# Optimization experiments

Measured on AMD Instinct MI355X. Metric: run time of the kernel, lower is better.

Reference implementation:

```python
import jax, jax.numpy as jnp
import numpy as np

B = 4
NS = [65536, 16384, 4096, 1024, 256]   # nodes per mesh level
DEG = 16                               # avg degree
KORD = 6                               # Chebyshev polynomial order
FE = [3, 16, 16, 16, 32]               # encoder filters
FD = [32, 16, 16, 16, 16, 3]           # decoder filters
Z = 64                                 # latent dim


def cheb_norm(edge_index, n):
    # symmetric normalization D^-1/2 A D^-1/2 per ChebConv_Coma.norm
    row, col = edge_index
    deg = jnp.zeros((n,), jnp.float32).at[row].add(jnp.ones(row.shape, jnp.float32))
    dis = jnp.where(deg > 0, deg ** -0.5, 0.0)
    return dis[row] * dis[col]


def propagate(x, row, col, norm):
    # out[b, row] += norm * x[b, col]   (sparse adjacency matvec, batched)
    return jnp.zeros_like(x).at[:, row].add(x[:, col] * norm[None, :, None])


def cheb_conv(x, edge_index, norm, W, b):
    # Chebyshev recursion: T0 = x, T1 = L x, Tk = 2 L T_{k-1} - T_{k-2}
    row, col = edge_index
    Tx0 = x
    out = jnp.einsum('bnf,fg->bng', Tx0, W[0])
    Tx1 = propagate(x, row, col, norm)
    out = out + jnp.einsum('bnf,fg->bng', Tx1, W[1])
    for k in range(2, W.shape[0]):
        Tx2 = 2.0 * propagate(Tx1, row, col, norm) - Tx0
        out = out + jnp.einsum('bnf,fg->bng', Tx2, W[k])
        Tx0, Tx1 = Tx1, Tx2
    return out + b if b is not None else out


def pool(x, idx, w):
    # sparse pooling matmul: 3 nnz per output row; idx/w: [Nout, 3]
    return jnp.einsum('bnkf,nk->bnf', x[:, idx], w)


def coma_forward(x, eis, dids, dws, uids, uws, encW, encB, decW, decB,
                 enc_w, enc_b, dec_w, dec_b):
    norms = [cheb_norm(eis[i], NS[i]) for i in range(5)]
    h = x.reshape(B, NS[0], FE[0])
    # encoder: cheb conv + relu + downsample pool, 4 levels
    for i in range(4):
        h = jax.nn.relu(cheb_conv(h, eis[i], norms[i], encW[i], encB[i]))
        h = pool(h, dids[i], dws[i])
    h = h.reshape(B, NS[-1] * FE[-1])
    z = jax.nn.relu(h @ enc_w + enc_b)
    # decoder
    h = jax.nn.relu(z @ dec_w + dec_b).reshape(B, NS[-1], FD[0])
    for i in range(4):
        lvl = 3 - i
        h = pool(h, uids[lvl], uws[lvl])
        h = jax.nn.relu(cheb_conv(h, eis[lvl], norms[lvl], decW[i], decB[i]))
    h = cheb_conv(h, eis[0], norms[0], decW[4], None)  # last conv, no bias
    return h.reshape(-1, FE[0])


def setup_inputs() -> dict:
    key = jax.random.key(0)
    ks = iter(jax.random.split(key, 80))
    inp = {}
    inp['x'] = jax.random.normal(next(ks), (B * NS[0], FE[0]), jnp.float32)
    for i, n in enumerate(NS):
        inp[f'ei{i}'] = jax.random.randint(next(ks), (2, DEG * n), 0, n)
    for i in range(4):
        inp[f'down_i{i}'] = jax.random.randint(next(ks), (NS[i + 1], 3), 0, NS[i])
        inp[f'down_w{i}'] = jax.random.uniform(next(ks), (NS[i + 1], 3), jnp.float32)
        inp[f'up_i{i}'] = jax.random.randint(next(ks), (NS[i], 3), 0, NS[i + 1])
        inp[f'up_w{i}'] = jax.random.uniform(next(ks), (NS[i], 3), jnp.float32)
    for i in range(4):
        inp[f'ew{i}'] = 0.1 * jax.random.normal(next(ks), (KORD, FE[i], FE[i + 1]), jnp.float32)
        inp[f'eb{i}'] = jnp.zeros((FE[i + 1],), jnp.float32)
    for i in range(5):
        inp[f'dw{i}'] = 0.1 * jax.random.normal(next(ks), (KORD, FD[i], FD[i + 1]), jnp.float32)
    for i in range(4):
        inp[f'db{i}'] = jnp.zeros((FD[i + 1],), jnp.float32)
    inp['enc_w'] = 0.1 * jax.random.normal(next(ks), (NS[-1] * FE[-1], Z), jnp.float32)
    inp['enc_b'] = 0.1 * jnp.ones((Z,), jnp.float32)
    inp['dec_w'] = 0.1 * jax.random.normal(next(ks), (Z, FD[0] * NS[-1]), jnp.float32)
    inp['dec_b'] = 0.1 * jnp.ones((FD[0] * NS[-1],), jnp.float32)
    return inp


def reference(x, ei0, ei1, ei2, ei3, ei4,
              down_i0, down_w0, up_i0, up_w0,
              down_i1, down_w1, up_i1, up_w1,
              down_i2, down_w2, up_i2, up_w2,
              down_i3, down_w3, up_i3, up_w3,
              ew0, eb0, ew1, eb1, ew2, eb2, ew3, eb3,
              dw0, dw1, dw2, dw3, dw4, db0, db1, db2, db3,
              enc_w, enc_b, dec_w, dec_b):
    eis = [ei0, ei1, ei2, ei3, ei4]
    dids = [down_i0, down_i1, down_i2, down_i3]
    dws = [down_w0, down_w1, down_w2, down_w3]
    uids = [up_i0, up_i1, up_i2, up_i3]
    uws = [up_w0, up_w1, up_w2, up_w3]
    encW = [ew0, ew1, ew2, ew3]
    encB = [eb0, eb1, eb2, eb3]
    decW = [dw0, dw1, dw2, dw3, dw4]
    decB = [db0, db1, db2, db3]
    return coma_forward(x, eis, dids, dws, uids, uws, encW, encB, decW, decB,
                        enc_w, enc_b, dec_w, dec_b)
```

## Files before the change

### kernel.cpp

```cpp
#include <hip/hip_runtime.h>

#define TPB 256

static constexpr int B_ = 4;
static constexpr int DEG_ = 16;

using u16 = unsigned short;

static constexpr int LB0 = 0, LB1 = 65536, LB2 = 81920, LB3 = 86016, LB4 = 87040;
static constexpr int CE0 = 0, CE1 = 1048576, CE2 = 1310720, CE3 = 1376256, CE4 = 1392640;


__device__ inline float b2f(u16 u) { return __uint_as_float((unsigned)u << 16); }
__device__ inline u16 f2b(float f) {
    unsigned b = __float_as_uint(f);
    b += 0x7fffu + ((b >> 16) & 1u);
    return (u16)(b >> 16);
}

template<int F>
__device__ inline void load_row_bf16(const u16* __restrict__ p, float* v) {
    if constexpr (F % 8 == 0) {
        #pragma unroll
        for (int i = 0; i < F / 8; ++i) {
            uint4 raw = reinterpret_cast<const uint4*>(p)[i];
            unsigned rr[4] = {raw.x, raw.y, raw.z, raw.w};
            #pragma unroll
            for (int k = 0; k < 4; ++k) {
                v[i * 8 + 2 * k]     = __uint_as_float(rr[k] << 16);
                v[i * 8 + 2 * k + 1] = __uint_as_float(rr[k] & 0xffff0000u);
            }
        }
    } else {
        #pragma unroll
        for (int f = 0; f < F; ++f) v[f] = b2f(p[f]);
    }
}

template<int F>
__device__ inline void store_row_bf16(u16* __restrict__ p, const float* v) {
    if constexpr (F % 8 == 0) {
        #pragma unroll
        for (int i = 0; i < F / 8; ++i) {
            uint4 raw;
            unsigned* rr = &raw.x;
            #pragma unroll
            for (int k = 0; k < 4; ++k)
                rr[k] = (unsigned)f2b(v[i * 8 + 2 * k]) |
                        ((unsigned)f2b(v[i * 8 + 2 * k + 1]) << 16);
            reinterpret_cast<uint4*>(p)[i] = raw;
        }
    } else {
        #pragma unroll
        for (int f = 0; f < F; ++f) p[f] = f2b(v[f]);
    }
}


__global__ void cnt_all_kernel(const int* __restrict__ r0, const int* __restrict__ r1,
                               const int* __restrict__ r2, const int* __restrict__ r3,
                               int* __restrict__ cntAll) {
    int e = blockIdx.x * blockDim.x + threadIdx.x;
    if (e >= CE4) return;
    const int* rp; int base, lb;
    if (e < CE1)      { rp = r0; base = CE0; lb = LB0; }
    else if (e < CE2) { rp = r1; base = CE1; lb = LB1; }
    else if (e < CE3) { rp = r2; base = CE2; lb = LB2; }
    else              { rp = r3; base = CE3; lb = LB3; }
    atomicAdd(&cntAll[lb + rp[e - base]], 1);
}

__global__ void scanA_kernel(const int* __restrict__ cnt, int* __restrict__ partial,
                             int* __restrict__ bsum) {
    __shared__ int sdata[256];
    int tid = threadIdx.x;
    int base = blockIdx.x * 1024 + tid * 4;
    int v0 = cnt[base], v1 = cnt[base + 1], v2 = cnt[base + 2], v3 = cnt[base + 3];
    int tsum = v0 + v1 + v2 + v3;
    sdata[tid] = tsum;
    __syncthreads();
    for (int ofs = 1; ofs < 256; ofs <<= 1) {
        int x = (tid >= ofs) ? sdata[tid - ofs] : 0;
        __syncthreads();
        sdata[tid] += x;
        __syncthreads();
    }
    int excl = sdata[tid] - tsum;
    partial[base] = excl;         excl += v0;
    partial[base + 1] = excl;     excl += v1;
    partial[base + 2] = excl;     excl += v2;
    partial[base + 3] = excl;
    if (tid == 255) bsum[blockIdx.x] = sdata[255];
}

__global__ void scanB_kernel(int* __restrict__ bsum, int nb) {
    __shared__ int s[128];
    int tid = threadIdx.x;
    int v = tid < nb ? bsum[tid] : 0;
    s[tid] = v;
    __syncthreads();
    for (int ofs = 1; ofs < 128; ofs <<= 1) {
        int x = (tid >= ofs) ? s[tid - ofs] : 0;
        __syncthreads();
        s[tid] += x;
        __syncthreads();
    }
    if (tid < nb) bsum[tid] = s[tid] - v;
}

__global__ void scanC_kernel(const int* __restrict__ partial, const int* __restrict__ bsum,
                             const int* __restrict__ cnt, float* __restrict__ disAll,
                             int* __restrict__ rp0, int* __restrict__ rp1,
                             int* __restrict__ rp2, int* __restrict__ rp3) {
    int i = blockIdx.x * blockDim.x + threadIdx.x;
    if (i >= LB4) return;
    int g = partial[i] + bsum[i >> 10];
    if (i < LB1)      rp0[i - LB0] = g - CE0;
    else if (i < LB2) rp1[i - LB1] = g - CE1;
    else if (i < LB3) rp2[i - LB2] = g - CE2;
    else              rp3[i - LB3] = g - CE3;
    int c = cnt[i];
    disAll[i] = c > 0 ? rsqrtf((float)c) : 0.f;
    if (i == 0) {
        rp0[LB1 - LB0] = CE1 - CE0;
        rp1[LB2 - LB1] = CE2 - CE1;
        rp2[LB3 - LB2] = CE3 - CE2;
        rp3[LB4 - LB3] = CE4 - CE3;
    }
}

__global__ void fill_all_kernel(const int* __restrict__ r0, const int* __restrict__ c0,
                                const int* __restrict__ r1, const int* __restrict__ c1,
                                const int* __restrict__ r2, const int* __restrict__ c2,
                                const int* __restrict__ r3, const int* __restrict__ c3,
                                const int* __restrict__ rp0, const int* __restrict__ rp1,
                                const int* __restrict__ rp2, const int* __restrict__ rp3,
                                int* __restrict__ curAll, u16* __restrict__ ccolAll) {
    int e = blockIdx.x * blockDim.x + threadIdx.x;
    if (e >= CE4) return;
    const int* rowp; const int* colp; const int* rptr; int base, lb;
    if (e < CE1)      { rowp = r0; colp = c0; rptr = rp0; base = CE0; lb = LB0; }
    else if (e < CE2) { rowp = r1; colp = c1; rptr = rp1; base = CE1; lb = LB1; }
    else if (e < CE3) { rowp = r2; colp = c2; rptr = rp2; base = CE2; lb = LB2; }
    else              { rowp = r3; colp = c3; rptr = rp3; base = CE3; lb = LB3; }
    int le = e - base;
    int r = rowp[le];
    int pos = rptr[r] + atomicAdd(&curAll[lb + r], 1);
    ccolAll[base + pos] = (u16)colp[le];
}


__global__ void f2b_tr_kernel(const float* __restrict__ in, u16* __restrict__ out, int N) {
    int t = blockIdx.x * blockDim.x + threadIdx.x;
    if (t >= B_ * N * 3) return;
    int f = t % 3;
    int nb = t / 3;
    int b = nb & 3;
    int n = nb >> 2;
    out[t] = f2b(in[((size_t)b * N + n) * 3 + f]);
}

template<int F, bool FIRST>
__global__ __launch_bounds__(128) void sweep_k(
    const u16* __restrict__ gsrc, const u16* __restrict__ selfp, u16* __restrict__ dst,
    const int* __restrict__ rowptr, const u16* __restrict__ ccol,
    const float* __restrict__ dis, int N)
{
    int t = blockIdx.x * 128 + (int)threadIdx.x;
    if (t >= B_ * N) return;
    int r = t >> 2;
    int b = t & 3;

    float tv[F];
    if constexpr (FIRST) {
        #pragma unroll
        for (int f = 0; f < F; ++f) tv[f] = 0.f;
    } else {
        float sv[F];
        load_row_bf16<F>(selfp + (size_t)t * F, sv);
        #pragma unroll
        for (int f = 0; f < F; ++f) tv[f] = -sv[f];
    }
    const float scale = (FIRST ? 1.0f : 2.0f) * dis[r];
    int beg = rowptr[r], end = rowptr[r + 1];
    for (int j = beg; j < end; ++j) {
        int c = (int)ccol[j];
        float w = scale * dis[c];
        float gv[F];
        load_row_bf16<F>(gsrc + (size_t)((c << 2) | b) * F, gv);
        #pragma unroll
        for (int f = 0; f < F; ++f) tv[f] += w * gv[f];
    }
    store_row_bf16<F>(dst + (size_t)t * F, tv);
}

template<int F, int G, bool OSTD>
__global__ __launch_bounds__(128) void combine_k(
    const u16* __restrict__ T0, const u16* __restrict__ T1, const u16* __restrict__ T2,
    const u16* __restrict__ T3, const u16* __restrict__ T4, const u16* __restrict__ T5,
    const float* __restrict__ W6, const float* __restrict__ bias,
    u16* __restrict__ outb, float* __restrict__ outf, int N, int relu)
{
    __shared__ float sW[6 * F * G];
    for (int i = threadIdx.x; i < 6 * F * G; i += 128) sW[i] = W6[i];
    __syncthreads();
    int t = blockIdx.x * 128 + (int)threadIdx.x;
    if (t >= B_ * N) return;

    float acc[G];
    #pragma unroll
    for (int g = 0; g < G; ++g) acc[g] = 0.f;

    const u16* Ts[6] = {T0, T1, T2, T3, T4, T5};
    #pragma unroll
    for (int k = 0; k < 6; ++k) {
        float tv[F];
        load_row_bf16<F>(Ts[k] + (size_t)t * F, tv);
        const float* w = sW + k * F * G;
        #pragma unroll
        for (int f = 0; f < F; ++f) {
            float x = tv[f];
            #pragma unroll
            for (int g = 0; g < G; ++g) acc[g] += x * w[f * G + g];
        }
    }
    if (bias) {
        #pragma unroll
        for (int g = 0; g < G; ++g) acc[g] += bias[g];
    }
    if (relu) {
        #pragma unroll
        for (int g = 0; g < G; ++g) acc[g] = fmaxf(acc[g], 0.f);
    }
    if (OSTD) {
        int r = t >> 2, b = t & 3;
        float* orow = outf + ((size_t)b * N + r) * G;
        #pragma unroll
        for (int g = 0; g < G; ++g) orow[g] = acc[g];
    } else {
        store_row_bf16<G>(outb + (size_t)t * G, acc);
    }
}


__global__ void pool_kernel(const u16* __restrict__ in, u16* __restrict__ out,
                            const int* __restrict__ idx, const float* __restrict__ w,
                            int Nout, int F) {
    int t = blockIdx.x * blockDim.x + threadIdx.x;
    if (t >= B_ * Nout * F) return;
    int f = t % F;
    int nb = t / F;
    int b = nb & 3;
    int n = nb >> 2;
    float acc = 0.f;
    for (int k = 0; k < 3; ++k) {
        int src = idx[n * 3 + k];
        acc += w[n * 3 + k] * b2f(in[(size_t)((src << 2) | b) * F + f]);
    }
    out[t] = f2b(acc);
}

__global__ void dense_enc_kernel(const u16* __restrict__ h, const float* __restrict__ W,
                                 const float* __restrict__ bias, float* __restrict__ z) {
    int b = blockIdx.x >> 6;
    int g = blockIdx.x & 63;
    int tid = threadIdx.x;
    float acc = 0.f;
    for (int i = tid; i < 8192; i += 256) {
        int n = i >> 5, f = i & 31;
        acc += b2f(h[(((size_t)n << 2) | b) * 32 + f]) * W[(size_t)i * 64 + g];
    }
    __shared__ float red[256];
    red[tid] = acc;
    __syncthreads();
    for (int sft = 128; sft > 0; sft >>= 1) {
        if (tid < sft) red[tid] += red[tid + sft];
        __syncthreads();
    }
    if (tid == 0) z[b * 64 + g] = fmaxf(red[0] + bias[g], 0.f);
}

__global__ void dense_dec_kernel(const float* __restrict__ z, const float* __restrict__ W,
                                 const float* __restrict__ bias, u16* __restrict__ out) {
    int t = blockIdx.x * blockDim.x + threadIdx.x;
    if (t >= B_ * 8192) return;
    int b = t / 8192, j = t % 8192;
    float acc = bias[j];
    for (int k = 0; k < 64; ++k) acc += z[b * 64 + k] * W[(size_t)k * 8192 + j];
    int n = j >> 5, f = j & 31;
    out[(((size_t)n << 2) | b) * 32 + f] = f2b(fmaxf(acc, 0.f));
}


static inline unsigned cdivu(size_t a, size_t b) { return (unsigned)((a + b - 1) / b); }

template<int F, int G, bool OSTD = false>
static void run_cheb(const u16* X, u16* const* T, const float* Wk, const float* bias,
                     int relu, u16* outb, float* outf,
                     const int* rp, const u16* cc, const float* dis, int N, hipStream_t s) {
    unsigned g = (unsigned)((size_t)B_ * N / 128);
    sweep_k<F, true><<<g, 128, 0, s>>>(X, nullptr, T[0], rp, cc, dis, N);
    sweep_k<F, false><<<g, 128, 0, s>>>(T[0], X, T[1], rp, cc, dis, N);
    sweep_k<F, false><<<g, 128, 0, s>>>(T[1], T[0], T[2], rp, cc, dis, N);
    sweep_k<F, false><<<g, 128, 0, s>>>(T[2], T[1], T[3], rp, cc, dis, N);
    sweep_k<F, false><<<g, 128, 0, s>>>(T[3], T[2], T[4], rp, cc, dis, N);
    combine_k<F, G, OSTD><<<g, 128, 0, s>>>(X, T[0], T[1], T[2], T[3], T[4],
                                            Wk, bias, outb, outf, N, relu);
}

extern "C" void kernel_launch(void* const* d_in, const int* in_sizes, int n_in,
                              void* d_out, int out_size, void* d_ws, size_t ws_size,
                              hipStream_t stream) {
    (void)in_sizes; (void)n_in; (void)out_size; (void)ws_size;
    hipStream_t s = stream;

    static const int NS_[5] = {65536, 16384, 4096, 1024, 256};
    static const int LBa[5] = {LB0, LB1, LB2, LB3, LB4};
    static const int CEa[5] = {CE0, CE1, CE2, CE3, CE4};

    const float* x = (const float*)d_in[0];
    const int* ei[4];
    for (int l = 0; l < 4; ++l) ei[l] = (const int*)d_in[1 + l];
    const int* down_i[4]; const float* down_w[4];
    const int* up_i[4];   const float* up_w[4];
    for (int i = 0; i < 4; ++i) {
        down_i[i] = (const int*)d_in[6 + 4 * i];
        down_w[i] = (const float*)d_in[7 + 4 * i];
        up_i[i]   = (const int*)d_in[8 + 4 * i];
        up_w[i]   = (const float*)d_in[9 + 4 * i];
    }
    const float* encW[4]; const float* encB[4];
    for (int i = 0; i < 4; ++i) {
        encW[i] = (const float*)d_in[22 + 2 * i];
        encB[i] = (const float*)d_in[23 + 2 * i];
    }
    const float* decW[5];
    for (int i = 0; i < 5; ++i) decW[i] = (const float*)d_in[30 + i];
    const float* decB[4];
    for (int i = 0; i < 4; ++i) decB[i] = (const float*)d_in[35 + i];
    const float* enc_w = (const float*)d_in[39];
    const float* enc_b = (const float*)d_in[40];
    const float* dec_w = (const float*)d_in[41];
    const float* dec_b = (const float*)d_in[42];

    float* ws = (float*)d_ws;
    size_t off = 0;
    const size_t HSLOT = (size_t)B_ * 65536 * 16 / 2;
    u16* XA = (u16*)(ws + off); off += HSLOT;
    u16* XB = (u16*)(ws + off); off += HSLOT;
    u16* T[5];
    for (int i = 0; i < 5; ++i) { T[i] = (u16*)(ws + off); off += HSLOT; }
    int* cntAll = (int*)(ws + off); off += LB4;
    int* curAll = (int*)(ws + off); off += LB4;
    int* partial = (int*)(ws + off); off += LB4;
    int* bsum = (int*)(ws + off); off += 128;
    float* disAll = ws + off; off += LB4;
    int* rowptr[4];
    for (int l = 0; l < 4; ++l) { rowptr[l] = (int*)(ws + off); off += (size_t)NS_[l] + 4; }
    u16* ccolAll = (u16*)(ws + off); off += (CE4 + 1) / 2;
    float* zbuf = ws + off; off += 256;

    hipMemsetAsync(cntAll, 0, (size_t)(2 * LB4) * sizeof(int), s);
    cnt_all_kernel<<<cdivu(CE4, TPB), TPB, 0, s>>>(ei[0], ei[1], ei[2], ei[3], cntAll);
    scanA_kernel<<<85, 256, 0, s>>>(cntAll, partial, bsum);
    scanB_kernel<<<1, 128, 0, s>>>(bsum, 85);
    scanC_kernel<<<cdivu(LB4, TPB), TPB, 0, s>>>(partial, bsum, cntAll, disAll,
                                                 rowptr[0], rowptr[1], rowptr[2], rowptr[3]);
    fill_all_kernel<<<cdivu(CE4, TPB), TPB, 0, s>>>(
        ei[0], ei[0] + DEG_ * NS_[0], ei[1], ei[1] + DEG_ * NS_[1],
        ei[2], ei[2] + DEG_ * NS_[2], ei[3], ei[3] + DEG_ * NS_[3],
        rowptr[0], rowptr[1], rowptr[2], rowptr[3], curAll, ccolAll);

    const float* dis[4]; const u16* cc[4];
    for (int l = 0; l < 4; ++l) { dis[l] = disAll + LBa[l]; cc[l] = ccolAll + CEa[l]; }

    f2b_tr_kernel<<<cdivu((size_t)B_ * 65536 * 3, TPB), TPB, 0, s>>>(x, XA, 65536);
    run_cheb<3, 16>(XA, T, encW[0], encB[0], 1, XB, nullptr,
                    rowptr[0], cc[0], dis[0], NS_[0], s);
    pool_kernel<<<cdivu((size_t)B_ * NS_[1] * 16, TPB), TPB, 0, s>>>(
        XB, XA, down_i[0], down_w[0], NS_[1], 16);
    run_cheb<16, 16>(XA, T, encW[1], encB[1], 1, XB, nullptr,
                     rowptr[1], cc[1], dis[1], NS_[1], s);
    pool_kernel<<<cdivu((size_t)B_ * NS_[2] * 16, TPB), TPB, 0, s>>>(
        XB, XA, down_i[1], down_w[1], NS_[2], 16);
    run_cheb<16, 16>(XA, T, encW[2], encB[2], 1, XB, nullptr,
                     rowptr[2], cc[2], dis[2], NS_[2], s);
    pool_kernel<<<cdivu((size_t)B_ * NS_[3] * 16, TPB), TPB, 0, s>>>(
        XB, XA, down_i[2], down_w[2], NS_[3], 16);
    run_cheb<16, 32>(XA, T, encW[3], encB[3], 1, XB, nullptr,
                     rowptr[3], cc[3], dis[3], NS_[3], s);
    pool_kernel<<<cdivu((size_t)B_ * NS_[4] * 32, TPB), TPB, 0, s>>>(
        XB, XA, down_i[3], down_w[3], NS_[4], 32);

    dense_enc_kernel<<<B_ * 64, 256, 0, s>>>(XA, enc_w, enc_b, zbuf);
    dense_dec_kernel<<<cdivu((size_t)B_ * 8192, TPB), TPB, 0, s>>>(zbuf, dec_w, dec_b, XB);

    pool_kernel<<<cdivu((size_t)B_ * NS_[3] * 32, TPB), TPB, 0, s>>>(
        XB, XA, up_i[3], up_w[3], NS_[3], 32);
    run_cheb<32, 16>(XA, T, decW[0], decB[0], 1, XB, nullptr,
                     rowptr[3], cc[3], dis[3], NS_[3], s);
    pool_kernel<<<cdivu((size_t)B_ * NS_[2] * 16, TPB), TPB, 0, s>>>(
        XB, XA, up_i[2], up_w[2], NS_[2], 16);
    run_cheb<16, 16>(XA, T, decW[1], decB[1], 1, XB, nullptr,
                     rowptr[2], cc[2], dis[2], NS_[2], s);
    pool_kernel<<<cdivu((size_t)B_ * NS_[1] * 16, TPB), TPB, 0, s>>>(
        XB, XA, up_i[1], up_w[1], NS_[1], 16);
    run_cheb<16, 16>(XA, T, decW[2], decB[2], 1, XB, nullptr,
                     rowptr[1], cc[1], dis[1], NS_[1], s);
    pool_kernel<<<cdivu((size_t)B_ * NS_[0] * 16, TPB), TPB, 0, s>>>(
        XB, XA, up_i[0], up_w[0], NS_[0], 16);
    run_cheb<16, 16>(XA, T, decW[3], decB[3], 1, XB, nullptr,
                     rowptr[0], cc[0], dis[0], NS_[0], s);
    run_cheb<16, 3, true>(XB, T, decW[4], nullptr, 0, nullptr, (float*)d_out,
                          rowptr[0], cc[0], dis[0], NS_[0], s);
}
```

Measured before the change: 1.117 ms.

## Use batch-major layout with per-batch block scheduling at finest mesh level

At level 0 the code now stores activations batch-major ([b][n][f]) instead of node-interleaved with batch, and adds sweep_p, which assigns each block one batch and a 128-node span. Blocks for the four batches are interleaved in launch order. Each batch's gather then reads a contiguous per-batch buffer, which may give better cache locality. New pool kernels convert between layouts at level boundaries. The input transpose and output transpose are dropped because the native layout now matches. The cost is that one neighbor's rows for the four batches are no longer adjacent in memory, so each edge gather touches separate cache lines per batch.

Measured after the change: 1.448 ms. 29.7% more time.

```diff
diff --git a/kernel.cpp b/kernel.cpp
--- a/kernel.cpp
+++ b/kernel.cpp
@@ -150,14 +150,46 @@
 }
 
 
-__global__ void f2b_tr_kernel(const float* __restrict__ in, u16* __restrict__ out, int N) {
-    int t = blockIdx.x * blockDim.x + threadIdx.x;
-    if (t >= B_ * N * 3) return;
-    int f = t % 3;
-    int nb = t / 3;
-    int b = nb & 3;
-    int n = nb >> 2;
-    out[t] = f2b(in[((size_t)b * N + n) * 3 + f]);
+__global__ void f2b_kernel(const float* __restrict__ in, u16* __restrict__ out, int n) {
+    int i = blockIdx.x * blockDim.x + threadIdx.x;
+    if (i < n) out[i] = f2b(in[i]);
+}
+
+template<int F, bool FIRST>
+__global__ __launch_bounds__(128) void sweep_p(
+    const u16* __restrict__ gsrc, const u16* __restrict__ selfp, u16* __restrict__ dst,
+    const int* __restrict__ rowptr, const u16* __restrict__ ccol,
+    const float* __restrict__ dis, int N)
+{
+    int blk = blockIdx.x;
+    int b = (blk >> 1) & 3;
+    int j = ((blk >> 3) << 1) | (blk & 1);
+    int r = j * 128 + (int)threadIdx.x;
+    if (r >= N) return;
+    size_t t = (size_t)b * N + r;
+
+    float tv[F];
+    if constexpr (FIRST) {
+        #pragma unroll
+        for (int f = 0; f < F; ++f) tv[f] = 0.f;
+    } else {
+        float sv[F];
+        load_row_bf16<F>(selfp + t * F, sv);
+        #pragma unroll
+        for (int f = 0; f < F; ++f) tv[f] = -sv[f];
+    }
+    const float scale = (FIRST ? 1.0f : 2.0f) * dis[r];
+    const u16* base = gsrc + (size_t)b * N * F;
+    int beg = rowptr[r], end = rowptr[r + 1];
+    for (int e = beg; e < end; ++e) {
+        int c = (int)ccol[e];
+        float w = scale * dis[c];
+        float gv[F];
+        load_row_bf16<F>(base + (size_t)c * F, gv);
+        #pragma unroll
+        for (int f = 0; f < F; ++f) tv[f] += w * gv[f];
+    }
+    store_row_bf16<F>(dst + t * F, tv);
 }
 
 template<int F, bool FIRST>
@@ -183,8 +215,8 @@
     }
     const float scale = (FIRST ? 1.0f : 2.0f) * dis[r];
     int beg = rowptr[r], end = rowptr[r + 1];
-    for (int j = beg; j < end; ++j) {
-        int c = (int)ccol[j];
+    for (int e = beg; e < end; ++e) {
+        int c = (int)ccol[e];
         float w = scale * dis[c];
         float gv[F];
         load_row_bf16<F>(gsrc + (size_t)((c << 2) | b) * F, gv);
@@ -233,8 +265,7 @@
         for (int g = 0; g < G; ++g) acc[g] = fmaxf(acc[g], 0.f);
     }
     if (OSTD) {
-        int r = t >> 2, b = t & 3;
-        float* orow = outf + ((size_t)b * N + r) * G;
+        float* orow = outf + (size_t)t * G;
         #pragma unroll
         for (int g = 0; g < G; ++g) orow[g] = acc[g];
     } else {
@@ -260,6 +291,40 @@
     out[t] = f2b(acc);
 }
 
+__global__ void pool_down0(const u16* __restrict__ in, u16* __restrict__ out,
+                           const int* __restrict__ idx, const float* __restrict__ w,
+                           int Nin, int Nout, int F) {
+    int t = blockIdx.x * blockDim.x + threadIdx.x;
+    if (t >= B_ * Nout * F) return;
+    int f = t % F;
+    int nb = t / F;
+    int b = nb & 3;
+    int n = nb >> 2;
+    float acc = 0.f;
+    for (int k = 0; k < 3; ++k) {
+        int src = idx[n * 3 + k];
+        acc += w[n * 3 + k] * b2f(in[((size_t)b * Nin + src) * F + f]);
+    }
+    out[t] = f2b(acc);
+}
+
+__global__ void pool_up0(const u16* __restrict__ in, u16* __restrict__ out,
+                         const int* __restrict__ idx, const float* __restrict__ w,
+                         int Nout, int F) {
+    int t = blockIdx.x * blockDim.x + threadIdx.x;
+    if (t >= B_ * Nout * F) return;
+    int f = t % F;
+    int bn = t / F;
+    int n = bn % Nout;
+    int b = bn / Nout;
+    float acc = 0.f;
+    for (int k = 0; k < 3; ++k) {
+        int src = idx[n * 3 + k];
+        acc += w[n * 3 + k] * b2f(in[(size_t)((src << 2) | b) * F + f]);
+    }
+    out[t] = f2b(acc);
+}
+
 __global__ void dense_enc_kernel(const u16* __restrict__ h, const float* __restrict__ W,
                                  const float* __restrict__ bias, float* __restrict__ z) {
     int b = blockIdx.x >> 6;
@@ -294,16 +359,30 @@
 
 static inline unsigned cdivu(size_t a, size_t b) { return (unsigned)((a + b - 1) / b); }
 
-template<int F, int G, bool OSTD = false>
+template<int F, int G>
 static void run_cheb(const u16* X, u16* const* T, const float* Wk, const float* bias,
-                     int relu, u16* outb, float* outf,
+                     int relu, u16* outb,
                      const int* rp, const u16* cc, const float* dis, int N, hipStream_t s) {
-    unsigned g = (unsigned)((size_t)B_ * N / 128);
+    unsigned g = (unsigned)cdivu((size_t)B_ * N, 128);
     sweep_k<F, true><<<g, 128, 0, s>>>(X, nullptr, T[0], rp, cc, dis, N);
     sweep_k<F, false><<<g, 128, 0, s>>>(T[0], X, T[1], rp, cc, dis, N);
     sweep_k<F, false><<<g, 128, 0, s>>>(T[1], T[0], T[2], rp, cc, dis, N);
     sweep_k<F, false><<<g, 128, 0, s>>>(T[2], T[1], T[3], rp, cc, dis, N);
     sweep_k<F, false><<<g, 128, 0, s>>>(T[3], T[2], T[4], rp, cc, dis, N);
+    combine_k<F, G, false><<<g, 128, 0, s>>>(X, T[0], T[1], T[2], T[3], T[4],
+                                             Wk, bias, outb, nullptr, N, relu);
+}
+
+template<int F, int G, bool OSTD = false>
+static void run_cheb_p(const u16* X, u16* const* T, const float* Wk, const float* bias,
+                       int relu, u16* outb, float* outf,
+                       const int* rp, const u16* cc, const float* dis, int N, hipStream_t s) {
+    unsigned g = (unsigned)cdivu((size_t)B_ * N, 128);
+    sweep_p<F, true><<<g, 128, 0, s>>>(X, nullptr, T[0], rp, cc, dis, N);
+    sweep_p<F, false><<<g, 128, 0, s>>>(T[0], X, T[1], rp, cc, dis, N);
+    sweep_p<F, false><<<g, 128, 0, s>>>(T[1], T[0], T[2], rp, cc, dis, N);
+    sweep_p<F, false><<<g, 128, 0, s>>>(T[2], T[1], T[3], rp, cc, dis, N);
+    sweep_p<F, false><<<g, 128, 0, s>>>(T[3], T[2], T[4], rp, cc, dis, N);
     combine_k<F, G, OSTD><<<g, 128, 0, s>>>(X, T[0], T[1], T[2], T[3], T[4],
                                             Wk, bias, outb, outf, N, relu);
 }
@@ -374,20 +453,20 @@
     const float* dis[4]; const u16* cc[4];
     for (int l = 0; l < 4; ++l) { dis[l] = disAll + LBa[l]; cc[l] = ccolAll + CEa[l]; }
 
-    f2b_tr_kernel<<<cdivu((size_t)B_ * 65536 * 3, TPB), TPB, 0, s>>>(x, XA, 65536);
-    run_cheb<3, 16>(XA, T, encW[0], encB[0], 1, XB, nullptr,
-                    rowptr[0], cc[0], dis[0], NS_[0], s);
-    pool_kernel<<<cdivu((size_t)B_ * NS_[1] * 16, TPB), TPB, 0, s>>>(
-        XB, XA, down_i[0], down_w[0], NS_[1], 16);
-    run_cheb<16, 16>(XA, T, encW[1], encB[1], 1, XB, nullptr,
+    f2b_kernel<<<cdivu((size_t)B_ * 65536 * 3, TPB), TPB, 0, s>>>(x, XA, B_ * 65536 * 3);
+    run_cheb_p<3, 16>(XA, T, encW[0], encB[0], 1, XB, nullptr,
+                      rowptr[0], cc[0], dis[0], NS_[0], s);
+    pool_down0<<<cdivu((size_t)B_ * NS_[1] * 16, TPB), TPB, 0, s>>>(
+        XB, XA, down_i[0], down_w[0], NS_[0], NS_[1], 16);
+    run_cheb<16, 16>(XA, T, encW[1], encB[1], 1, XB,
                      rowptr[1], cc[1], dis[1], NS_[1], s);
     pool_kernel<<<cdivu((size_t)B_ * NS_[2] * 16, TPB), TPB, 0, s>>>(
         XB, XA, down_i[1], down_w[1], NS_[2], 16);
-    run_cheb<16, 16>(XA, T, encW[2], encB[2], 1, XB, nullptr,
+    run_cheb<16, 16>(XA, T, encW[2], encB[2], 1, XB,
                      rowptr[2], cc[2], dis[2], NS_[2], s);
     pool_kernel<<<cdivu((size_t)B_ * NS_[3] * 16, TPB), TPB, 0, s>>>(
         XB, XA, down_i[2], down_w[2], NS_[3], 16);
-    run_cheb<16, 32>(XA, T, encW[3], encB[3], 1, XB, nullptr,
+    run_cheb<16, 32>(XA, T, encW[3], encB[3], 1, XB,
                      rowptr[3], cc[3], dis[3], NS_[3], s);
     pool_kernel<<<cdivu((size_t)B_ * NS_[4] * 32, TPB), TPB, 0, s>>>(
         XB, XA, down_i[3], down_w[3], NS_[4], 32);
@@ -397,20 +476,20 @@
 
     pool_kernel<<<cdivu((size_t)B_ * NS_[3] * 32, TPB), TPB, 0, s>>>(
         XB, XA, up_i[3], up_w[3], NS_[3], 32);
-    run_cheb<32, 16>(XA, T, decW[0], decB[0], 1, XB, nullptr,
+    run_cheb<32, 16>(XA, T, decW[0], decB[0], 1, XB,
                      rowptr[3], cc[3], dis[3], NS_[3], s);
     pool_kernel<<<cdivu((size_t)B_ * NS_[2] * 16, TPB), TPB, 0, s>>>(
         XB, XA, up_i[2], up_w[2], NS_[2], 16);
-    run_cheb<16, 16>(XA, T, decW[1], decB[1], 1, XB, nullptr,
+    run_cheb<16, 16>(XA, T, decW[1], decB[1], 1, XB,
                      rowptr[2], cc[2], dis[2], NS_[2], s);
     pool_kernel<<<cdivu((size_t)B_ * NS_[1] * 16, TPB), TPB, 0, s>>>(
         XB, XA, up_i[1], up_w[1], NS_[1], 16);
-    run_cheb<16, 16>(XA, T, decW[2], decB[2], 1, XB, nullptr,
+    run_cheb<16, 16>(XA, T, decW[2], decB[2], 1, XB,
                      rowptr[1], cc[1], dis[1], NS_[1], s);
-    pool_kernel<<<cdivu((size_t)B_ * NS_[0] * 16, TPB), TPB, 0, s>>>(
+    pool_up0<<<cdivu((size_t)B_ * NS_[0] * 16, TPB), TPB, 0, s>>>(
         XB, XA, up_i[0], up_w[0], NS_[0], 16);
-    run_cheb<16, 16>(XA, T, decW[3], decB[3], 1, XB, nullptr,
-                     rowptr[0], cc[0], dis[0], NS_[0], s);
-    run_cheb<16, 3, true>(XB, T, decW[4], nullptr, 0, nullptr, (float*)d_out,
-                          rowptr[0], cc[0], dis[0], NS_[0], s);
-}
+    run_cheb_p<16, 16>(XA, T, decW[3], decB[3], 1, XB, nullptr,
+                       rowptr[0], cc[0], dis[0], NS_[0], s);
+    run_cheb_p<16, 3, true>(XB, T, decW[4], nullptr, 0, nullptr, (float*)d_out,
+                            rowptr[0], cc[0], dis[0], NS_[0], s);
+}
```
